# Performance work log

Hardware: AMD Instinct MI355X
Metric: run time of the kernel (lower is better)

The kernel has to match this reference:

```python
import jax, jax.numpy as jnp
import numpy as np

B, S, D = 1024, 256, 256  # batch, n_class, feature dim (g = n_component = 1)


def setup_inputs() -> dict:
    key = jax.random.key(0)
    k1, k2, k3 = jax.random.split(key, 3)
    x = jax.random.normal(k1, (B, D), dtype=jnp.float32)
    mu_p = jax.random.normal(k2, (S, 1, D), dtype=jnp.float32)
    sigma_p = jax.random.normal(k3, (S, 1, D, D), dtype=jnp.float32)
    return {"x": x, "mu_p": mu_p, "sigma_p": sigma_p}


def _log_probs(x, mu_p, sigma_p):
    sp = sigma_p[:, 0]            # (S, D, D), component index g=0
    mu = mu_p[:, 0]               # (S, D)
    # parameter_enforcing: m = sigma_p^T @ sigma_p (PSD);
    # mean of (real) eigenvalues of m == trace(m)/D, so the ridge term is
    # 0.01 * (trace(m)/D) * I, making sigma symmetric positive definite.
    m = jnp.einsum('skd,ske->sde', sp, sp)                      # (S, D, D)
    ridge = 0.01 * (jnp.trace(m, axis1=-2, axis2=-1) / D)       # (S,)
    sigma = m + ridge[:, None, None] * jnp.eye(D, dtype=m.dtype)
    # MVN log_prob via Cholesky: logdet = 2*sum(log diag L),
    # maha = || L^{-1} (x - mu) ||^2
    L = jnp.linalg.cholesky(sigma)                              # (S, D, D)
    logdet = 2.0 * jnp.sum(jnp.log(jnp.diagonal(L, axis1=-2, axis2=-1)), -1)  # (S,)
    diff = x[None, :, :] - mu[:, None, :]                       # (S, B, D)
    # batched triangular solve per class: y = L^{-1} diff^T -> (S, D, B)
    y = jax.vmap(lambda Ls, ds: jax.scipy.linalg.solve_triangular(Ls, ds.T, lower=True))(L, diff)
    maha = jnp.sum(y * y, axis=1)                               # (S, B)
    log2pi = jnp.log(2.0 * jnp.pi).astype(x.dtype)
    logp = -0.5 * (D * log2pi + logdet[:, None] + maha)         # (S, B)
    return logp.T                                               # (B, S)


def reference(x, mu_p, sigma_p):
    return _log_probs(x, mu_p, sigma_p)
```

## Files before the change

### kernel.cpp

```cpp
#include <hip/hip_runtime.h>
#include <math.h>


#define LOG2PI_D 470.4965290007924f

typedef __attribute__((ext_vector_type(8))) short bf16x8;
typedef __attribute__((ext_vector_type(4))) float f32x4;

__device__ __forceinline__ unsigned bf16rtn(float f) {
  unsigned u = __float_as_uint(f);
  return (u + 0x7FFFu + ((u >> 16) & 1u)) >> 16;
}
__device__ __forceinline__ unsigned packhl(float v) {
  unsigned h = bf16rtn(v);
  float hf = __uint_as_float(h << 16);
  unsigned l = bf16rtn(v - hf);
  return (h << 16) | l;
}

__global__ __launch_bounds__(256) void k_gram(const float* __restrict__ sp,
                                              float* __restrict__ L,
                                              float* __restrict__ ridge_out) {
  __shared__ unsigned Hb[4 * 128 * 20];
  unsigned* AH = Hb;
  unsigned* AL = Hb + 128 * 20;
  unsigned* BH = Hb + 2 * 128 * 20;
  unsigned* BL = Hb + 3 * 128 * 20;
  int p = blockIdx.y, s = blockIdx.x;
  int bi = (p ? 128 : 0), bj = (p == 2 ? 128 : 0);
  const float* A = sp + (size_t)s * 65536;
  float* C = L + (size_t)s * 65536;
  int tid = threadIdx.x, w = tid >> 6, lane = tid & 63;
  int q = lane >> 4, n = lane & 15;
  int mt_[2] = {w, 7 - w};
  f32x4 acc[2][8] = {};
  int c = tid & 127, g = tid >> 7;

  float va[16], vb[16];
#pragma unroll
  for (int u = 0; u < 16; ++u) {
    va[u] = A[(size_t)(g * 16 + u) * 256 + bi + c];
    if (p == 1) vb[u] = A[(size_t)(g * 16 + u) * 256 + bj + c];
  }

  for (int ks = 0; ks < 8; ++ks) {
    __syncthreads();
    {
      unsigned hw[8], lw[8];
#pragma unroll
      for (int m = 0; m < 8; ++m) {
        float v0 = va[2 * m], v1 = va[2 * m + 1];
        unsigned h0 = bf16rtn(v0), h1 = bf16rtn(v1);
        float r0 = v0 - __uint_as_float(h0 << 16);
        float r1 = v1 - __uint_as_float(h1 << 16);
        hw[m] = h0 | (h1 << 16);
        lw[m] = bf16rtn(r0) | (bf16rtn(r1) << 16);
      }
      *(uint4*)&AH[c * 20 + g * 8] = make_uint4(hw[0], hw[1], hw[2], hw[3]);
      *(uint4*)&AH[c * 20 + g * 8 + 4] = make_uint4(hw[4], hw[5], hw[6], hw[7]);
      *(uint4*)&AL[c * 20 + g * 8] = make_uint4(lw[0], lw[1], lw[2], lw[3]);
      *(uint4*)&AL[c * 20 + g * 8 + 4] = make_uint4(lw[4], lw[5], lw[6], lw[7]);
      if (p == 1) {
#pragma unroll
        for (int m = 0; m < 8; ++m) {
          float v0 = vb[2 * m], v1 = vb[2 * m + 1];
          unsigned h0 = bf16rtn(v0), h1 = bf16rtn(v1);
          float r0 = v0 - __uint_as_float(h0 << 16);
          float r1 = v1 - __uint_as_float(h1 << 16);
          hw[m] = h0 | (h1 << 16);
          lw[m] = bf16rtn(r0) | (bf16rtn(r1) << 16);
        }
        *(uint4*)&BH[c * 20 + g * 8] = make_uint4(hw[0], hw[1], hw[2], hw[3]);
        *(uint4*)&BH[c * 20 + g * 8 + 4] = make_uint4(hw[4], hw[5], hw[6], hw[7]);
        *(uint4*)&BL[c * 20 + g * 8] = make_uint4(lw[0], lw[1], lw[2], lw[3]);
        *(uint4*)&BL[c * 20 + g * 8 + 4] = make_uint4(lw[4], lw[5], lw[6], lw[7]);
      }
    }
    __syncthreads();
    if (ks < 7) {
      int r0g = (ks + 1) * 32 + g * 16;
#pragma unroll
      for (int u = 0; u < 16; ++u) {
        va[u] = A[(size_t)(r0g + u) * 256 + bi + c];
        if (p == 1) vb[u] = A[(size_t)(r0g + u) * 256 + bj + c];
      }
    }
    const unsigned* TBH = (p == 1) ? BH : AH;
    const unsigned* TBL = (p == 1) ? BL : AL;
    bf16x8 Ah[2], Al[2];
#pragma unroll
    for (int t = 0; t < 2; ++t) {
      int col = mt_[t] * 16 + n;
      Ah[t] = *(const bf16x8*)&AH[col * 20 + q * 4];
      Al[t] = *(const bf16x8*)&AL[col * 20 + q * 4];
    }
    int ntmax = (p == 1) ? 8 : (8 - w);
    for (int nt = 0; nt < ntmax; ++nt) {
      bf16x8 bh = *(const bf16x8*)&TBH[(nt * 16 + n) * 20 + q * 4];
      bf16x8 bl = *(const bf16x8*)&TBL[(nt * 16 + n) * 20 + q * 4];
#pragma unroll
      for (int t = 0; t < 2; ++t) {
        if (p == 1 || nt <= mt_[t]) {
          acc[t][nt] = __builtin_amdgcn_mfma_f32_16x16x32_bf16(Ah[t], bh, acc[t][nt], 0, 0, 0);
          acc[t][nt] = __builtin_amdgcn_mfma_f32_16x16x32_bf16(Ah[t], bl, acc[t][nt], 0, 0, 0);
          acc[t][nt] = __builtin_amdgcn_mfma_f32_16x16x32_bf16(Al[t], bh, acc[t][nt], 0, 0, 0);
        }
      }
    }
  }
  if (p != 1) {
    float dsum = 0.f;
#pragma unroll
    for (int t = 0; t < 2; ++t) {
      if ((n >> 2) == q) dsum += acc[t][mt_[t]][n & 3];
    }
    dsum += __shfl_down(dsum, 32, 64);
    dsum += __shfl_down(dsum, 16, 64);
    dsum += __shfl_down(dsum, 8, 64);
    dsum += __shfl_down(dsum, 4, 64);
    dsum += __shfl_down(dsum, 2, 64);
    dsum += __shfl_down(dsum, 1, 64);
    if (lane == 0) atomicAdd(&ridge_out[s], dsum * (0.01f / 256.0f));
  }
  float* slab = (float*)Hb;
  for (int t = 0; t < 2; ++t) {
    __syncthreads();
#pragma unroll
    for (int nt = 0; nt < 8; ++nt)
#pragma unroll
      for (int r = 0; r < 4; ++r)
        slab[w * 2048 + (q * 4 + r) * 128 + nt * 16 + n] = acc[t][nt][r];
    __syncthreads();
#pragma unroll
    for (int it = 0; it < 8; ++it) {
      int idx = tid + it * 256;
      int row = idx >> 5, c4 = idx & 31;
      int wsrc = row >> 4, r16 = row & 15;
      int rt = t ? (7 - wsrc) : wsrc;
      if (p == 1 || (c4 >> 2) <= rt) {
        int d = bi + rt * 16 + r16;
        *(float4*)(C + (size_t)d * 256 + bj + c4 * 4) =
            *(float4*)&slab[wsrc * 2048 + r16 * 128 + c4 * 4];
      }
    }
  }
}

__global__ __launch_bounds__(512) void k_factor(float* __restrict__ L,
                                                const float* __restrict__ ridge_buf) {
  extern __shared__ float lds[];
  float* P = lds;
  float* W = lds + 64 * 68;
  float* WT = lds + 2 * 64 * 68;
  float* T = lds + 3 * 64 * 68;
  float* T2 = lds + 4 * 64 * 68;
  int s = blockIdx.x;
  float* M = L + (size_t)s * 65536;
  unsigned* M32 = (unsigned*)M;
  int tid = threadIdx.x;
  int k4 = tid & 15, rb = tid >> 4;
  float ridge = ridge_buf[s];

  for (int kb = 0; kb < 4; ++kb) {
    int base = kb * 64;
    __syncthreads();
    for (int r = rb; r < 64; r += 16)
      *(float4*)&P[r * 68 + k4 * 4] = *(const float4*)(M + (size_t)(base + r) * 256 + base + k4 * 4);
    __syncthreads();
    if (tid < 64) P[tid * 68 + tid] += ridge;
    __syncthreads();
    {
      int eo = tid & 63, ro = tid >> 6;
      for (int cb = 0; cb < 16; ++cb) {
        int c0 = cb * 4;
        float g00 = P[c0 * 68 + c0];
        float g10 = P[(c0 + 1) * 68 + c0], g11 = P[(c0 + 1) * 68 + c0 + 1];
        float g20 = P[(c0 + 2) * 68 + c0], g21 = P[(c0 + 2) * 68 + c0 + 1],
              g22 = P[(c0 + 2) * 68 + c0 + 2];
        float g30 = P[(c0 + 3) * 68 + c0], g31 = P[(c0 + 3) * 68 + c0 + 1],
              g32 = P[(c0 + 3) * 68 + c0 + 2], g33 = P[(c0 + 3) * 68 + c0 + 3];
        float l00 = sqrtf(g00), r0 = 1.f / l00;
        float l10 = g10 * r0, l20 = g20 * r0, l30 = g30 * r0;
        float l11 = sqrtf(g11 - l10 * l10), r1 = 1.f / l11;
        float l21 = (g21 - l20 * l10) * r1, l31 = (g31 - l30 * l10) * r1;
        float l22 = sqrtf(g22 - l20 * l20 - l21 * l21), r2 = 1.f / l22;
        float l32 = (g32 - l30 * l20 - l31 * l21) * r2;
        float l33 = sqrtf(g33 - l30 * l30 - l31 * l31 - l32 * l32), r3 = 1.f / l33;
        int e = c0 + 4 + eo;
        if (e < 64) {
          float p0 = P[e * 68 + c0], p1 = P[e * 68 + c0 + 1];
          float p2 = P[e * 68 + c0 + 2], p3 = P[e * 68 + c0 + 3];
          float le0 = p0 * r0;
          float le1 = (p1 - le0 * l10) * r1;
          float le2 = (p2 - le0 * l20 - le1 * l21) * r2;
          float le3 = (p3 - le0 * l30 - le1 * l31 - le2 * l32) * r3;
          for (int r = c0 + 4 + ro; r < 64; r += 8) {
            float q0 = P[r * 68 + c0], q1 = P[r * 68 + c0 + 1];
            float q2 = P[r * 68 + c0 + 2], q3 = P[r * 68 + c0 + 3];
            float lr0 = q0 * r0;
            float lr1 = (q1 - lr0 * l10) * r1;
            float lr2 = (q2 - lr0 * l20 - lr1 * l21) * r2;
            float lr3 = (q3 - lr0 * l30 - lr1 * l31 - lr2 * l32) * r3;
            P[r * 68 + e] -= lr0 * le0 + lr1 * le1 + lr2 * le2 + lr3 * le3;
          }
        }
        __syncthreads();
      }
    }
    {
      int cb = tid >> 4, lane16 = tid & 15;
      int c0 = cb * 4;
      float vals[4][4];
      int rows[4], nr = 0;
      if (tid < 256) {
        float g00 = P[c0 * 68 + c0];
        float g10 = P[(c0 + 1) * 68 + c0], g11 = P[(c0 + 1) * 68 + c0 + 1];
        float g20 = P[(c0 + 2) * 68 + c0], g21 = P[(c0 + 2) * 68 + c0 + 1],
              g22 = P[(c0 + 2) * 68 + c0 + 2];
        float g30 = P[(c0 + 3) * 68 + c0], g31 = P[(c0 + 3) * 68 + c0 + 1],
              g32 = P[(c0 + 3) * 68 + c0 + 2], g33 = P[(c0 + 3) * 68 + c0 + 3];
        float l00 = sqrtf(g00), r0 = 1.f / l00;
        float l10 = g10 * r0, l20 = g20 * r0, l30 = g30 * r0;
        float l11 = sqrtf(g11 - l10 * l10), r1 = 1.f / l11;
        float l21 = (g21 - l20 * l10) * r1, l31 = (g31 - l30 * l10) * r1;
        float l22 = sqrtf(g22 - l20 * l20 - l21 * l21), r2 = 1.f / l22;
        float l32 = (g32 - l30 * l20 - l31 * l21) * r2;
        float l33 = sqrtf(g33 - l30 * l30 - l31 * l31 - l32 * l32), r3 = 1.f / l33;
        for (int r = c0 + lane16; r < 64; r += 16) {
          int i = r - c0;
          if (i == 0) { vals[nr][0] = l00; vals[nr][1] = 0; vals[nr][2] = 0; vals[nr][3] = 0; }
          else if (i == 1) { vals[nr][0] = l10; vals[nr][1] = l11; vals[nr][2] = 0; vals[nr][3] = 0; }
          else if (i == 2) { vals[nr][0] = l20; vals[nr][1] = l21; vals[nr][2] = l22; vals[nr][3] = 0; }
          else if (i == 3) { vals[nr][0] = l30; vals[nr][1] = l31; vals[nr][2] = l32; vals[nr][3] = l33; }
          else {
            float q0 = P[r * 68 + c0], q1 = P[r * 68 + c0 + 1];
            float q2 = P[r * 68 + c0 + 2], q3 = P[r * 68 + c0 + 3];
            float lr0 = q0 * r0;
            float lr1 = (q1 - lr0 * l10) * r1;
            float lr2 = (q2 - lr0 * l20 - lr1 * l21) * r2;
            float lr3 = (q3 - lr0 * l30 - lr1 * l31 - lr2 * l32) * r3;
            vals[nr][0] = lr0; vals[nr][1] = lr1; vals[nr][2] = lr2; vals[nr][3] = lr3;
          }
          rows[nr++] = r;
        }
      }
      __syncthreads();
      if (tid < 256) {
        for (int u = 0; u < nr; ++u) {
          int r = rows[u];
          P[r * 68 + c0] = vals[u][0];
          P[r * 68 + c0 + 1] = vals[u][1];
          P[r * 68 + c0 + 2] = vals[u][2];
          P[r * 68 + c0 + 3] = vals[u][3];
        }
      }
    }
    __syncthreads();
    for (int idx = tid; idx < 64 * 68; idx += 512) W[idx] = 0.f;
    __syncthreads();
    for (int rb4 = 0; rb4 < 16; ++rb4) {
      int k0 = rb4 * 4;
      if (tid < 256) {
        int i = tid >> 6, cc = tid & 63;
        int row = k0 + i;
        float ssum = 0.f;
        for (int k = 0; k < k0; ++k) ssum += P[row * 68 + k] * W[k * 68 + cc];
        WT[i * 68 + cc] = ssum;
      }
      __syncthreads();
      if (tid < 64) {
        int cc = tid;
        float d00 = P[(k0 + 0) * 68 + k0];
        float d10 = P[(k0 + 1) * 68 + k0], d11 = P[(k0 + 1) * 68 + k0 + 1];
        float d20 = P[(k0 + 2) * 68 + k0], d21 = P[(k0 + 2) * 68 + k0 + 1],
              d22 = P[(k0 + 2) * 68 + k0 + 2];
        float d30 = P[(k0 + 3) * 68 + k0], d31 = P[(k0 + 3) * 68 + k0 + 1],
              d32 = P[(k0 + 3) * 68 + k0 + 2], d33 = P[(k0 + 3) * 68 + k0 + 3];
        float e0 = (cc == k0) ? 1.f : 0.f, e1 = (cc == k0 + 1) ? 1.f : 0.f;
        float e2 = (cc == k0 + 2) ? 1.f : 0.f, e3 = (cc == k0 + 3) ? 1.f : 0.f;
        float x0 = (e0 - WT[0 * 68 + cc]) / d00;
        float x1 = (e1 - WT[1 * 68 + cc] - d10 * x0) / d11;
        float x2 = (e2 - WT[2 * 68 + cc] - d20 * x0 - d21 * x1) / d22;
        float x3 = (e3 - WT[3 * 68 + cc] - d30 * x0 - d31 * x1 - d32 * x2) / d33;
        W[(k0 + 0) * 68 + cc] = x0;
        W[(k0 + 1) * 68 + cc] = x1;
        W[(k0 + 2) * 68 + cc] = x2;
        W[(k0 + 3) * 68 + cc] = x3;
      }
      __syncthreads();
    }
    for (int c = rb; c < 64; c += 16) {
      float4 v = *(float4*)&W[c * 68 + k4 * 4];
      WT[(k4 * 4 + 0) * 68 + c] = v.x;
      WT[(k4 * 4 + 1) * 68 + c] = v.y;
      WT[(k4 * 4 + 2) * 68 + c] = v.z;
      WT[(k4 * 4 + 3) * 68 + c] = v.w;
    }
    __syncthreads();
    for (int r = rb; r < 64; r += 16)
      *(float4*)(M + (size_t)(base + r) * 256 + base + k4 * 4) = *(float4*)&W[r * 68 + k4 * 4];
    int nrt = 3 - kb;
    for (int rt0 = 0; rt0 < nrt; rt0 += 2) {
      int pr = tid >> 8, t2 = tid & 255;
      int my = rt0 + pr;
      bool act = my < nrt;
      float* Tb = pr ? T2 : T;
      int k42 = t2 & 15, rb2 = t2 >> 4;
      int ty2 = t2 >> 4, tx2 = t2 & 15;
      int g0 = base + 64 + my * 64;
      __syncthreads();
      if (act) {
        for (int r = rb2; r < 64; r += 16) {
          float4 v = *(const float4*)(M + (size_t)(g0 + r) * 256 + base + k42 * 4);
          Tb[(k42 * 4 + 0) * 68 + r] = v.x;
          Tb[(k42 * 4 + 1) * 68 + r] = v.y;
          Tb[(k42 * 4 + 2) * 68 + r] = v.z;
          Tb[(k42 * 4 + 3) * 68 + r] = v.w;
        }
      }
      __syncthreads();
      float acc[4][4] = {};
      if (act) {
        for (int k = 0; k < 64; ++k) {
          float a[4], b[4];
          *(float4*)a = *(float4*)&Tb[k * 68 + ty2 * 4];
          *(float4*)b = *(float4*)&WT[k * 68 + tx2 * 4];
#pragma unroll
          for (int i = 0; i < 4; ++i)
#pragma unroll
            for (int j = 0; j < 4; ++j) acc[i][j] += a[i] * b[j];
        }
      }
      __syncthreads();
      if (act) {
#pragma unroll
        for (int i = 0; i < 4; ++i)
          *(float4*)(M + (size_t)(g0 + ty2 * 4 + i) * 256 + base + tx2 * 4) =
              make_float4(acc[i][0], acc[i][1], acc[i][2], acc[i][3]);
#pragma unroll
        for (int i = 0; i < 4; ++i)
#pragma unroll
          for (int j = 0; j < 4; ++j) Tb[(tx2 * 4 + j) * 68 + ty2 * 4 + i] = acc[i][j];
      }
      __syncthreads();
      if (act) {
        for (int r = rb2; r < 64; r += 16)
          *(float4*)(M + (size_t)(base + r) * 256 + g0 + k42 * 4) = *(float4*)&Tb[r * 68 + k42 * 4];
      }
    }
    int np = ((3 - kb) * (4 - kb)) / 2;
    for (int p0 = 0; p0 < np; p0 += 2) {
      int pr = tid >> 8, t2 = tid & 255;
      int my = p0 + pr;
      bool act = my < np;
      int ti = 1, tj = 1;
      {
        int cnt = 0;
        for (int a = kb + 1; a < 4; ++a)
          for (int b = kb + 1; b <= a; ++b) {
            if (cnt == my) { ti = a; tj = b; }
            ++cnt;
          }
      }
      float* Pi = pr ? WT : P;
      float* Pj = pr ? T : W;
      int k42 = t2 & 15, rb2 = t2 >> 4;
      int ty2 = t2 >> 4, tx2 = t2 & 15;
      __syncthreads();
      float acc[4][4];
      if (act) {
        for (int k = rb2; k < 64; k += 16) {
          *(float4*)&Pi[k * 68 + k42 * 4] =
              *(const float4*)(M + (size_t)(base + k) * 256 + ti * 64 + k42 * 4);
          *(float4*)&Pj[k * 68 + k42 * 4] =
              *(const float4*)(M + (size_t)(base + k) * 256 + tj * 64 + k42 * 4);
        }
#pragma unroll
        for (int i = 0; i < 4; ++i)
          *(float4*)&acc[i][0] =
              *(const float4*)(M + (size_t)(ti * 64 + ty2 * 4 + i) * 256 + tj * 64 + tx2 * 4);
      }
      __syncthreads();
      if (act) {
        for (int k = 0; k < 64; ++k) {
          float a[4], b[4];
          *(float4*)a = *(float4*)&Pi[k * 68 + ty2 * 4];
          *(float4*)b = *(float4*)&Pj[k * 68 + tx2 * 4];
#pragma unroll
          for (int i = 0; i < 4; ++i)
#pragma unroll
            for (int j = 0; j < 4; ++j) acc[i][j] -= a[i] * b[j];
        }
#pragma unroll
        for (int i = 0; i < 4; ++i)
          *(float4*)(M + (size_t)(ti * 64 + ty2 * 4 + i) * 256 + tj * 64 + tx2 * 4) =
              make_float4(acc[i][0], acc[i][1], acc[i][2], acc[i][3]);
      }
    }
  }

  {
    float* Bcol = lds;
    float* LW = lds + 3 * 64 * 68;
    float* Cs = lds + 4 * 64 * 68;
    int ty = tid >> 4, tx = tid & 15;
    for (int j = 0; j < 3; ++j) {
      __syncthreads();
      for (int r = rb; r < 64; r += 16)
        *(float4*)&Bcol[r * 68 + k4 * 4] =
            *(const float4*)(M + (size_t)(j * 64 + r) * 256 + j * 64 + k4 * 4);
      __syncthreads();

      for (int i = j + 1; i < 4; ++i) {
        float acc[4][4] = {};
        for (int kk = j; kk < i; ++kk) {
          __syncthreads();
          for (int k = rb; k < 64; k += 16)
            *(float4*)&LW[k * 68 + k4 * 4] =
                *(const float4*)(M + (size_t)(kk * 64 + k) * 256 + i * 64 + k4 * 4);
          __syncthreads();
          float* Bk = Bcol + (kk - j) * 64 * 68;
          if (tid < 256) {
#pragma unroll 4
            for (int k = 0; k < 64; ++k) {
              float a[4], b[4];
              *(float4*)a = *(float4*)&LW[k * 68 + ty * 4];
              *(float4*)b = *(float4*)&Bk[k * 68 + tx * 4];
#pragma unroll
              for (int r = 0; r < 4; ++r)
#pragma unroll
                for (int cc = 0; cc < 4; ++cc) acc[r][cc] += a[r] * b[cc];
            }
          }
        }
        __syncthreads();
        if (tid < 256) {
#pragma unroll
          for (int r = 0; r < 4; ++r)
            *(float4*)&Cs[(ty * 4 + r) * 68 + tx * 4] =
                make_float4(acc[r][0], acc[r][1], acc[r][2], acc[r][3]);
        }
        for (int r = rb; r < 64; r += 16) {
          float4 v = *(const float4*)(M + (size_t)(i * 64 + r) * 256 + i * 64 + k4 * 4);
          LW[(k4 * 4 + 0) * 68 + r] = v.x;
          LW[(k4 * 4 + 1) * 68 + r] = v.y;
          LW[(k4 * 4 + 2) * 68 + r] = v.z;
          LW[(k4 * 4 + 3) * 68 + r] = v.w;
        }
        __syncthreads();
        if (tid < 256) {
          float d[4][4] = {};
#pragma unroll 4
          for (int k = 0; k < 64; ++k) {
            float a[4], b[4];
            *(float4*)a = *(float4*)&LW[k * 68 + ty * 4];
            *(float4*)b = *(float4*)&Cs[k * 68 + tx * 4];
#pragma unroll
            for (int r = 0; r < 4; ++r)
#pragma unroll
              for (int cc = 0; cc < 4; ++cc) d[r][cc] -= a[r] * b[cc];
          }
          float* Bi = Bcol + (i - j) * 64 * 68;
#pragma unroll
          for (int r = 0; r < 4; ++r) {
            if (i < 3)
              *(float4*)&Bi[(ty * 4 + r) * 68 + tx * 4] =
                  make_float4(d[r][0], d[r][1], d[r][2], d[r][3]);
            uint4 pu;
            pu.x = packhl(d[r][0]); pu.y = packhl(d[r][1]);
            pu.z = packhl(d[r][2]); pu.w = packhl(d[r][3]);
            *(uint4*)(M32 + (size_t)(i * 64 + ty * 4 + r) * 256 + j * 64 + tx * 4) = pu;
          }
        }
        __syncthreads();
      }
    }
  }
}

__global__ __launch_bounds__(512) void k_maha(const float* __restrict__ x,
                                              const float* __restrict__ mu_p,
                                              const float* __restrict__ Lw,
                                              float* __restrict__ out) {
  __shared__ __align__(16) short Bh[128 * 40];
  __shared__ __align__(16) short Bl[128 * 40];
  __shared__ float Red[1025];
  int s = blockIdx.x, b0 = blockIdx.y * 128;
  const float* Mf = Lw + (size_t)s * 65536;
  const unsigned* M32 = (const unsigned*)Mf;
  int tid = threadIdx.x, w = tid >> 6, lane = tid & 63;
  int q = lane >> 4, n = lane & 15;
  int mt_[2] = {w, 15 - w};
  f32x4 acc[2][8] = {};

  for (int ks = 0; ks < 8; ++ks) {
    __syncthreads();
    {
      int b = tid >> 2, q8 = tid & 3;
      const float* xp = x + (size_t)(b0 + b) * 256 + ks * 32 + q8 * 8;
      const float* mp = mu_p + (size_t)s * 256 + ks * 32 + q8 * 8;
      float4 xa = ((const float4*)xp)[0], xb = ((const float4*)xp)[1];
      float4 ma = ((const float4*)mp)[0], mb = ((const float4*)mp)[1];
      float dv[8] = {xa.x - ma.x, xa.y - ma.y, xa.z - ma.z, xa.w - ma.w,
                     xb.x - mb.x, xb.y - mb.y, xb.z - mb.z, xb.w - mb.w};
      unsigned h[8], l[8];
#pragma unroll
      for (int jj = 0; jj < 8; ++jj) {
        h[jj] = bf16rtn(dv[jj]);
        float hf = __uint_as_float(h[jj] << 16);
        l[jj] = bf16rtn(dv[jj] - hf);
      }
      *(uint4*)&Bh[b * 40 + q8 * 8] =
          make_uint4(h[0] | (h[1] << 16), h[2] | (h[3] << 16),
                     h[4] | (h[5] << 16), h[6] | (h[7] << 16));
      *(uint4*)&Bl[b * 40 + q8 * 8] =
          make_uint4(l[0] | (l[1] << 16), l[2] | (l[3] << 16),
                     l[4] | (l[5] << 16), l[6] | (l[7] << 16));
    }
    __syncthreads();
    bf16x8 Ah[2], Al[2];
    bool act[2];
#pragma unroll
    for (int t = 0; t < 2; ++t) {
      int mt = mt_[t];
      act[t] = ks < ((mt + 2) >> 1);
      if (act[t]) {
        const unsigned* ap = M32 + (size_t)(mt * 16 + n) * 256 + ks * 32 + q * 8;
        uint4 u0 = *(const uint4*)ap;
        uint4 u1 = *(const uint4*)(ap + 4);
        unsigned uu[8] = {u0.x, u0.y, u0.z, u0.w, u1.x, u1.y, u1.z, u1.w};
        if ((ks >> 1) == (mt >> 2)) {
#pragma unroll
          for (int jj = 0; jj < 8; ++jj) {
            float f = __uint_as_float(uu[jj]);
            unsigned hh = bf16rtn(f);
            float hf = __uint_as_float(hh << 16);
            Ah[t][jj] = (short)hh;
            Al[t][jj] = (short)bf16rtn(f - hf);
          }
        } else {
#pragma unroll
          for (int jj = 0; jj < 8; ++jj) {
            Ah[t][jj] = (short)(uu[jj] >> 16);
            Al[t][jj] = (short)(uu[jj] & 0xffffu);
          }
        }
      }
    }
#pragma unroll
    for (int bsub = 0; bsub < 8; ++bsub) {
      bf16x8 bh = *(const bf16x8*)&Bh[(bsub * 16 + n) * 40 + q * 8];
      bf16x8 bl = *(const bf16x8*)&Bl[(bsub * 16 + n) * 40 + q * 8];
#pragma unroll
      for (int t = 0; t < 2; ++t) {
        if (act[t]) {
          acc[t][bsub] = __builtin_amdgcn_mfma_f32_16x16x32_bf16(Ah[t], bh, acc[t][bsub], 0, 0, 0);
          acc[t][bsub] = __builtin_amdgcn_mfma_f32_16x16x32_bf16(Ah[t], bl, acc[t][bsub], 0, 0, 0);
          acc[t][bsub] = __builtin_amdgcn_mfma_f32_16x16x32_bf16(Al[t], bh, acc[t][bsub], 0, 0, 0);
        }
      }
    }
  }
#pragma unroll
  for (int bsub = 0; bsub < 8; ++bsub) {
    float v = 0.f;
#pragma unroll
    for (int t = 0; t < 2; ++t)
#pragma unroll
      for (int r = 0; r < 4; ++r) v += acc[t][bsub][r] * acc[t][bsub][r];
    v += __shfl_xor(v, 16, 64);
    v += __shfl_xor(v, 32, 64);
    if (lane < 16) Red[w * 128 + bsub * 16 + lane] = v;
  }
  if (w == 0) {
    float ld = 0.f;
#pragma unroll
    for (int c = 0; c < 4; ++c)
      ld += logf(Mf[(size_t)(c * 64 + lane) * 256 + c * 64 + lane]);
    ld += __shfl_down(ld, 32, 64);
    ld += __shfl_down(ld, 16, 64);
    ld += __shfl_down(ld, 8, 64);
    ld += __shfl_down(ld, 4, 64);
    ld += __shfl_down(ld, 2, 64);
    ld += __shfl_down(ld, 1, 64);
    if (lane == 0) Red[1024] = ld;
  }
  __syncthreads();
  if (tid < 128) {
    float mh = 0.f;
#pragma unroll
    for (int w2 = 0; w2 < 8; ++w2) mh += Red[w2 * 128 + tid];
    out[(size_t)(b0 + tid) * 256 + s] = -0.5f * (LOG2PI_D - 2.0f * Red[1024] + mh);
  }
}

extern "C" void kernel_launch(void* const* d_in, const int* in_sizes, int n_in,
                              void* d_out, int out_size, void* d_ws, size_t ws_size,
                              hipStream_t stream) {
  const float* x = (const float*)d_in[0];
  const float* mu = (const float*)d_in[1];
  const float* sp = (const float*)d_in[2];
  float* out = (float*)d_out;
  float* L = (float*)d_ws;

  const int fact_lds = 5 * 64 * 68 * 4;
  (void)hipFuncSetAttribute((const void*)k_factor,
                            hipFuncAttributeMaxDynamicSharedMemorySize, fact_lds);

  k_gram<<<dim3(256, 3), 256, 0, stream>>>(sp, L, out);
  k_factor<<<256, 512, fact_lds, stream>>>(L, out);
  k_maha<<<dim3(256, 8), 512, 0, stream>>>(x, mu, L, out);
}
```

Measured before the change: 614.7 us.

## Split off-diagonal inverse into separate kernel and widen factor block to 1024 threads

Moves the block-column inverse computation out of k_factor into a new k_invcol kernel launched over (class, column) pairs, so the three column computations run in parallel across blocks instead of serially inside one block that left half its threads idle. k_factor now uses 1024 threads with smaller per-thread tiles (2x4) and a reduced LDS footprint, reusing the P buffer for the trailing-panel staging. The change adds an extra kernel launch and a global-memory round trip for the factored blocks, and lowers per-thread register reuse in the GEMM-like updates.

```diff
diff --git a/kernel.cpp b/kernel.cpp
--- a/kernel.cpp
+++ b/kernel.cpp
@@ -146,26 +146,24 @@
   }
 }
 
-__global__ __launch_bounds__(512) void k_factor(float* __restrict__ L,
-                                                const float* __restrict__ ridge_buf) {
+__global__ __launch_bounds__(1024) void k_factor(float* __restrict__ L,
+                                                 const float* __restrict__ ridge_buf) {
   extern __shared__ float lds[];
   float* P = lds;
   float* W = lds + 64 * 68;
   float* WT = lds + 2 * 64 * 68;
   float* T = lds + 3 * 64 * 68;
-  float* T2 = lds + 4 * 64 * 68;
   int s = blockIdx.x;
   float* M = L + (size_t)s * 65536;
-  unsigned* M32 = (unsigned*)M;
   int tid = threadIdx.x;
-  int k4 = tid & 15, rb = tid >> 4;
+  int k4 = tid & 15, r64 = tid >> 4;
   float ridge = ridge_buf[s];
 
   for (int kb = 0; kb < 4; ++kb) {
     int base = kb * 64;
     __syncthreads();
-    for (int r = rb; r < 64; r += 16)
-      *(float4*)&P[r * 68 + k4 * 4] = *(const float4*)(M + (size_t)(base + r) * 256 + base + k4 * 4);
+    *(float4*)&P[r64 * 68 + k4 * 4] =
+        *(const float4*)(M + (size_t)(base + r64) * 256 + base + k4 * 4);
     __syncthreads();
     if (tid < 64) P[tid * 68 + tid] += ridge;
     __syncthreads();
@@ -194,7 +192,7 @@
           float le1 = (p1 - le0 * l10) * r1;
           float le2 = (p2 - le0 * l20 - le1 * l21) * r2;
           float le3 = (p3 - le0 * l30 - le1 * l31 - le2 * l32) * r3;
-          for (int r = c0 + 4 + ro; r < 64; r += 8) {
+          for (int r = c0 + 4 + ro; r < 64; r += 16) {
             float q0 = P[r * 68 + c0], q1 = P[r * 68 + c0 + 1];
             float q2 = P[r * 68 + c0 + 2], q3 = P[r * 68 + c0 + 3];
             float lr0 = q0 * r0;
@@ -256,7 +254,7 @@
       }
     }
     __syncthreads();
-    for (int idx = tid; idx < 64 * 68; idx += 512) W[idx] = 0.f;
+    for (int idx = tid; idx < 64 * 68; idx += 1024) W[idx] = 0.f;
     __syncthreads();
     for (int rb4 = 0; rb4 < 16; ++rb4) {
       int k0 = rb4 * 4;
@@ -289,28 +287,28 @@
       }
       __syncthreads();
     }
-    for (int c = rb; c < 64; c += 16) {
-      float4 v = *(float4*)&W[c * 68 + k4 * 4];
-      WT[(k4 * 4 + 0) * 68 + c] = v.x;
-      WT[(k4 * 4 + 1) * 68 + c] = v.y;
-      WT[(k4 * 4 + 2) * 68 + c] = v.z;
-      WT[(k4 * 4 + 3) * 68 + c] = v.w;
-    }
-    __syncthreads();
-    for (int r = rb; r < 64; r += 16)
-      *(float4*)(M + (size_t)(base + r) * 256 + base + k4 * 4) = *(float4*)&W[r * 68 + k4 * 4];
+    {
+      float4 v = *(float4*)&W[r64 * 68 + k4 * 4];
+      WT[(k4 * 4 + 0) * 68 + r64] = v.x;
+      WT[(k4 * 4 + 1) * 68 + r64] = v.y;
+      WT[(k4 * 4 + 2) * 68 + r64] = v.z;
+      WT[(k4 * 4 + 3) * 68 + r64] = v.w;
+    }
+    __syncthreads();
+    *(float4*)(M + (size_t)(base + r64) * 256 + base + k4 * 4) = *(float4*)&W[r64 * 68 + k4 * 4];
     int nrt = 3 - kb;
     for (int rt0 = 0; rt0 < nrt; rt0 += 2) {
-      int pr = tid >> 8, t2 = tid & 255;
+      int pr = tid >> 9, t2 = tid & 511;
       int my = rt0 + pr;
       bool act = my < nrt;
-      float* Tb = pr ? T2 : T;
-      int k42 = t2 & 15, rb2 = t2 >> 4;
+      float* Tb = pr ? T : P;
+      int k42 = t2 & 15, rbl = t2 >> 4;
       int ty2 = t2 >> 4, tx2 = t2 & 15;
       int g0 = base + 64 + my * 64;
       __syncthreads();
       if (act) {
-        for (int r = rb2; r < 64; r += 16) {
+#pragma unroll
+        for (int r = rbl; r < 64; r += 32) {
           float4 v = *(const float4*)(M + (size_t)(g0 + r) * 256 + base + k42 * 4);
           Tb[(k42 * 4 + 0) * 68 + r] = v.x;
           Tb[(k42 * 4 + 1) * 68 + r] = v.y;
@@ -319,38 +317,40 @@
         }
       }
       __syncthreads();
-      float acc[4][4] = {};
+      float acc[2][4] = {};
       if (act) {
         for (int k = 0; k < 64; ++k) {
-          float a[4], b[4];
-          *(float4*)a = *(float4*)&Tb[k * 68 + ty2 * 4];
+          float a0 = Tb[k * 68 + ty2 * 2], a1 = Tb[k * 68 + ty2 * 2 + 1];
+          float b[4];
           *(float4*)b = *(float4*)&WT[k * 68 + tx2 * 4];
 #pragma unroll
-          for (int i = 0; i < 4; ++i)
-#pragma unroll
-            for (int j = 0; j < 4; ++j) acc[i][j] += a[i] * b[j];
+          for (int j = 0; j < 4; ++j) {
+            acc[0][j] += a0 * b[j];
+            acc[1][j] += a1 * b[j];
+          }
         }
       }
       __syncthreads();
       if (act) {
 #pragma unroll
-        for (int i = 0; i < 4; ++i)
-          *(float4*)(M + (size_t)(g0 + ty2 * 4 + i) * 256 + base + tx2 * 4) =
+        for (int i = 0; i < 2; ++i)
+          *(float4*)(M + (size_t)(g0 + ty2 * 2 + i) * 256 + base + tx2 * 4) =
               make_float4(acc[i][0], acc[i][1], acc[i][2], acc[i][3]);
 #pragma unroll
-        for (int i = 0; i < 4; ++i)
-#pragma unroll
-          for (int j = 0; j < 4; ++j) Tb[(tx2 * 4 + j) * 68 + ty2 * 4 + i] = acc[i][j];
+        for (int i = 0; i < 2; ++i)
+#pragma unroll
+          for (int j = 0; j < 4; ++j) Tb[(tx2 * 4 + j) * 68 + ty2 * 2 + i] = acc[i][j];
       }
       __syncthreads();
       if (act) {
-        for (int r = rb2; r < 64; r += 16)
+#pragma unroll
+        for (int r = rbl; r < 64; r += 32)
           *(float4*)(M + (size_t)(base + r) * 256 + g0 + k42 * 4) = *(float4*)&Tb[r * 68 + k42 * 4];
       }
     }
     int np = ((3 - kb) * (4 - kb)) / 2;
     for (int p0 = 0; p0 < np; p0 += 2) {
-      int pr = tid >> 8, t2 = tid & 255;
+      int pr = tid >> 9, t2 = tid & 511;
       int my = p0 + pr;
       bool act = my < np;
       int ti = 1, tj = 1;
@@ -364,117 +364,116 @@
       }
       float* Pi = pr ? WT : P;
       float* Pj = pr ? T : W;
-      int k42 = t2 & 15, rb2 = t2 >> 4;
+      int k42 = t2 & 15, rbl = t2 >> 4;
       int ty2 = t2 >> 4, tx2 = t2 & 15;
       __syncthreads();
-      float acc[4][4];
+      float acc[2][4];
       if (act) {
-        for (int k = rb2; k < 64; k += 16) {
+#pragma unroll
+        for (int k = rbl; k < 64; k += 32) {
           *(float4*)&Pi[k * 68 + k42 * 4] =
               *(const float4*)(M + (size_t)(base + k) * 256 + ti * 64 + k42 * 4);
           *(float4*)&Pj[k * 68 + k42 * 4] =
               *(const float4*)(M + (size_t)(base + k) * 256 + tj * 64 + k42 * 4);
         }
 #pragma unroll
-        for (int i = 0; i < 4; ++i)
+        for (int i = 0; i < 2; ++i)
           *(float4*)&acc[i][0] =
-              *(const float4*)(M + (size_t)(ti * 64 + ty2 * 4 + i) * 256 + tj * 64 + tx2 * 4);
+              *(const float4*)(M + (size_t)(ti * 64 + ty2 * 2 + i) * 256 + tj * 64 + tx2 * 4);
       }
       __syncthreads();
       if (act) {
         for (int k = 0; k < 64; ++k) {
-          float a[4], b[4];
-          *(float4*)a = *(float4*)&Pi[k * 68 + ty2 * 4];
+          float a0 = Pi[k * 68 + ty2 * 2], a1 = Pi[k * 68 + ty2 * 2 + 1];
+          float b[4];
           *(float4*)b = *(float4*)&Pj[k * 68 + tx2 * 4];
 #pragma unroll
-          for (int i = 0; i < 4; ++i)
-#pragma unroll
-            for (int j = 0; j < 4; ++j) acc[i][j] -= a[i] * b[j];
-        }
-#pragma unroll
-        for (int i = 0; i < 4; ++i)
-          *(float4*)(M + (size_t)(ti * 64 + ty2 * 4 + i) * 256 + tj * 64 + tx2 * 4) =
+          for (int j = 0; j < 4; ++j) {
+            acc[0][j] -= a0 * b[j];
+            acc[1][j] -= a1 * b[j];
+          }
+        }
+#pragma unroll
+        for (int i = 0; i < 2; ++i)
+          *(float4*)(M + (size_t)(ti * 64 + ty2 * 2 + i) * 256 + tj * 64 + tx2 * 4) =
               make_float4(acc[i][0], acc[i][1], acc[i][2], acc[i][3]);
       }
     }
   }
-
-  {
-    float* Bcol = lds;
-    float* LW = lds + 3 * 64 * 68;
-    float* Cs = lds + 4 * 64 * 68;
-    int ty = tid >> 4, tx = tid & 15;
-    for (int j = 0; j < 3; ++j) {
-      __syncthreads();
-      for (int r = rb; r < 64; r += 16)
-        *(float4*)&Bcol[r * 68 + k4 * 4] =
-            *(const float4*)(M + (size_t)(j * 64 + r) * 256 + j * 64 + k4 * 4);
-      __syncthreads();
-
-      for (int i = j + 1; i < 4; ++i) {
-        float acc[4][4] = {};
-        for (int kk = j; kk < i; ++kk) {
-          __syncthreads();
-          for (int k = rb; k < 64; k += 16)
-            *(float4*)&LW[k * 68 + k4 * 4] =
-                *(const float4*)(M + (size_t)(kk * 64 + k) * 256 + i * 64 + k4 * 4);
-          __syncthreads();
-          float* Bk = Bcol + (kk - j) * 64 * 68;
-          if (tid < 256) {
+}
+
+__global__ __launch_bounds__(256) void k_invcol(float* __restrict__ Lw) {
+  extern __shared__ float lds[];
+  float* Bcol = lds;
+  float* LW = lds + 3 * 64 * 68;
+  float* Cs = LW + 64 * 68;
+  int j = blockIdx.y, s = blockIdx.x;
+  float* M = Lw + (size_t)s * 65536;
+  unsigned* M32 = (unsigned*)M;
+  int tid = threadIdx.x, k4 = tid & 15, rb = tid >> 4;
+  int ty = tid >> 4, tx = tid & 15;
+
+  for (int r = rb; r < 64; r += 16)
+    *(float4*)&Bcol[r * 68 + k4 * 4] =
+        *(const float4*)(M + (size_t)(j * 64 + r) * 256 + j * 64 + k4 * 4);
+  __syncthreads();
+
+  for (int i = j + 1; i < 4; ++i) {
+    float acc[4][4] = {};
+    for (int kk = j; kk < i; ++kk) {
+      __syncthreads();
+      for (int k = rb; k < 64; k += 16)
+        *(float4*)&LW[k * 68 + k4 * 4] =
+            *(const float4*)(M + (size_t)(kk * 64 + k) * 256 + i * 64 + k4 * 4);
+      __syncthreads();
+      float* Bk = Bcol + (kk - j) * 64 * 68;
 #pragma unroll 4
-            for (int k = 0; k < 64; ++k) {
-              float a[4], b[4];
-              *(float4*)a = *(float4*)&LW[k * 68 + ty * 4];
-              *(float4*)b = *(float4*)&Bk[k * 68 + tx * 4];
-#pragma unroll
-              for (int r = 0; r < 4; ++r)
-#pragma unroll
-                for (int cc = 0; cc < 4; ++cc) acc[r][cc] += a[r] * b[cc];
-            }
-          }
-        }
-        __syncthreads();
-        if (tid < 256) {
-#pragma unroll
-          for (int r = 0; r < 4; ++r)
-            *(float4*)&Cs[(ty * 4 + r) * 68 + tx * 4] =
-                make_float4(acc[r][0], acc[r][1], acc[r][2], acc[r][3]);
-        }
-        for (int r = rb; r < 64; r += 16) {
-          float4 v = *(const float4*)(M + (size_t)(i * 64 + r) * 256 + i * 64 + k4 * 4);
-          LW[(k4 * 4 + 0) * 68 + r] = v.x;
-          LW[(k4 * 4 + 1) * 68 + r] = v.y;
-          LW[(k4 * 4 + 2) * 68 + r] = v.z;
-          LW[(k4 * 4 + 3) * 68 + r] = v.w;
-        }
-        __syncthreads();
-        if (tid < 256) {
-          float d[4][4] = {};
+      for (int k = 0; k < 64; ++k) {
+        float a[4], b[4];
+        *(float4*)a = *(float4*)&LW[k * 68 + ty * 4];
+        *(float4*)b = *(float4*)&Bk[k * 68 + tx * 4];
+#pragma unroll
+        for (int r = 0; r < 4; ++r)
+#pragma unroll
+          for (int c = 0; c < 4; ++c) acc[r][c] += a[r] * b[c];
+      }
+    }
+    __syncthreads();
+#pragma unroll
+    for (int r = 0; r < 4; ++r)
+      *(float4*)&Cs[(ty * 4 + r) * 68 + tx * 4] =
+          make_float4(acc[r][0], acc[r][1], acc[r][2], acc[r][3]);
+    for (int r = rb; r < 64; r += 16) {
+      float4 v = *(const float4*)(M + (size_t)(i * 64 + r) * 256 + i * 64 + k4 * 4);
+      LW[(k4 * 4 + 0) * 68 + r] = v.x;
+      LW[(k4 * 4 + 1) * 68 + r] = v.y;
+      LW[(k4 * 4 + 2) * 68 + r] = v.z;
+      LW[(k4 * 4 + 3) * 68 + r] = v.w;
+    }
+    __syncthreads();
+    float d[4][4] = {};
 #pragma unroll 4
-          for (int k = 0; k < 64; ++k) {
-            float a[4], b[4];
-            *(float4*)a = *(float4*)&LW[k * 68 + ty * 4];
-            *(float4*)b = *(float4*)&Cs[k * 68 + tx * 4];
-#pragma unroll
-            for (int r = 0; r < 4; ++r)
-#pragma unroll
-              for (int cc = 0; cc < 4; ++cc) d[r][cc] -= a[r] * b[cc];
-          }
-          float* Bi = Bcol + (i - j) * 64 * 68;
-#pragma unroll
-          for (int r = 0; r < 4; ++r) {
-            if (i < 3)
-              *(float4*)&Bi[(ty * 4 + r) * 68 + tx * 4] =
-                  make_float4(d[r][0], d[r][1], d[r][2], d[r][3]);
-            uint4 pu;
-            pu.x = packhl(d[r][0]); pu.y = packhl(d[r][1]);
-            pu.z = packhl(d[r][2]); pu.w = packhl(d[r][3]);
-            *(uint4*)(M32 + (size_t)(i * 64 + ty * 4 + r) * 256 + j * 64 + tx * 4) = pu;
-          }
-        }
-        __syncthreads();
-      }
-    }
+    for (int k = 0; k < 64; ++k) {
+      float a[4], b[4];
+      *(float4*)a = *(float4*)&LW[k * 68 + ty * 4];
+      *(float4*)b = *(float4*)&Cs[k * 68 + tx * 4];
+#pragma unroll
+      for (int r = 0; r < 4; ++r)
+#pragma unroll
+        for (int c = 0; c < 4; ++c) d[r][c] -= a[r] * b[c];
+    }
+    float* Bi = Bcol + (i - j) * 64 * 68;
+#pragma unroll
+    for (int r = 0; r < 4; ++r) {
+      if (i < 3)
+        *(float4*)&Bi[(ty * 4 + r) * 68 + tx * 4] =
+            make_float4(d[r][0], d[r][1], d[r][2], d[r][3]);
+      uint4 pu;
+      pu.x = packhl(d[r][0]); pu.y = packhl(d[r][1]);
+      pu.z = packhl(d[r][2]); pu.w = packhl(d[r][3]);
+      *(uint4*)(M32 + (size_t)(i * 64 + ty * 4 + r) * 256 + j * 64 + tx * 4) = pu;
+    }
+    __syncthreads();
   }
 }
 
@@ -603,11 +602,15 @@
   float* out = (float*)d_out;
   float* L = (float*)d_ws;
 
-  const int fact_lds = 5 * 64 * 68 * 4;
+  const int fact_lds = 4 * 64 * 68 * 4;
+  const int invc_lds = 5 * 64 * 68 * 4;
   (void)hipFuncSetAttribute((const void*)k_factor,
                             hipFuncAttributeMaxDynamicSharedMemorySize, fact_lds);
+  (void)hipFuncSetAttribute((const void*)k_invcol,
+                            hipFuncAttributeMaxDynamicSharedMemorySize, invc_lds);
 
   k_gram<<<dim3(256, 3), 256, 0, stream>>>(sp, L, out);
-  k_factor<<<256, 512, fact_lds, stream>>>(L, out);
+  k_factor<<<256, 1024, fact_lds, stream>>>(L, out);
+  k_invcol<<<dim3(256, 3), 256, invc_lds, stream>>>(L);
   k_maha<<<dim3(256, 8), 512, 0, stream>>>(x, mu, L, out);
 }
```

Measured after the change: 645.7 us. 1.05x slower.
